# Performance work log

Measured on AMD Instinct MI355X. Metric: run time of the kernel, lower is better.

## Reference

```python
import jax, jax.numpy as jnp
import numpy as np

LAMBDA_COORD = 5.0
LAMBDA_NOOBJ = 0.5
CELL_SILE = 1.0 / 7.0


def setup_inputs() -> dict:
    key = jax.random.key(0)
    k1, k2, k3 = jax.random.split(key, 3)
    B, S, C = 16384, 49, 30
    predictions = jax.random.normal(k1, (B, S, C), dtype=jnp.float32)
    targets = jax.random.uniform(k2, (B, S, C), dtype=jnp.float32)
    # confidence column must be exactly 0/1 for the equality masks in the loss
    obj = (jax.random.uniform(k3, (B, S)) < 0.3).astype(jnp.float32)
    targets = targets.at[:, :, 4].set(obj)
    return {"predictions": predictions, "targets": targets}


def reference(predictions, targets):
    # Flatten cells: row-major order matches torch boolean indexing order.
    p = predictions.reshape(-1, 30)  # [N, 30], N = B*49
    t = targets.reshape(-1, 30)
    conf = t[:, 4]
    coord_mask = conf == 1.0
    noobj = (conf == 0.0).astype(p.dtype)

    # no-object confidence loss on columns [4, 9]
    noobj_loss = LAMBDA_NOOBJ * jnp.sum(
        noobj * ((p[:, 4] - t[:, 4]) ** 2 + (p[:, 9] - t[:, 9]) ** 2))

    # The original zips N_obj rows against N_obj//2 output rows, so only the
    # first floor(N_obj/2) object cells (in flattened order) contribute.
    n_obj = jnp.sum(coord_mask.astype(jnp.int32))
    rank = jnp.cumsum(coord_mask.astype(jnp.int32))  # 1-indexed object rank
    w = (coord_mask & (rank <= n_obj // 2)).astype(p.dtype)

    # pred boxes: columns [0:4] and [5:9] -> [N, 2, 4]
    pb = p[:, :10].reshape(-1, 2, 5)[..., :4]
    # faithful in-place transform: a = xy*c - wh ; b = a*c + wh
    pa = pb[..., :2] * CELL_SILE - pb[..., 2:4]
    pbb = pa * CELL_SILE + pb[..., 2:4]
    pbox = jnp.concatenate([pa, pbb], axis=-1)  # [N, 2, 4]

    tb = jnp.square(t[:, :4])
    ta = tb[:, :2] * CELL_SILE - tb[:, 2:4]
    tbb = ta * CELL_SILE + tb[:, 2:4]
    tbox = jnp.concatenate([ta, tbb], axis=-1)  # [N, 4]

    # torchvision.ops.box_iou, batched over cells
    lt = jnp.maximum(pbox[..., :2], tbox[:, None, :2])
    rb = jnp.minimum(pbox[..., 2:], tbox[:, None, 2:])
    whd = jnp.clip(rb - lt, 0.0)
    inter = whd[..., 0] * whd[..., 1]  # [N, 2]
    area_p = (pbox[..., 2] - pbox[..., 0]) * (pbox[..., 3] - pbox[..., 1])
    area_t = (tbox[:, 2] - tbox[:, 0]) * (tbox[:, 3] - tbox[:, 1])
    iou = inter / (area_p + area_t[:, None] - inter)  # [N, 2]

    idx = jnp.argmax(iou, axis=1)  # responsible box per cell
    sel = jnp.take_along_axis(p[:, :10].reshape(-1, 2, 5),
                              idx[:, None, None], axis=1)[:, 0, :]  # [N, 5]
    obj_idx = jnp.argmax(t[:, 10:], axis=1)
    sel_cls = jnp.take_along_axis(p[:, 10:], obj_idx[:, None], axis=1)[:, 0]

    center = jnp.sum(w * jnp.sum((sel[:, :2] - t[:, :2]) ** 2, axis=1))
    xywh = jnp.sum(w * jnp.sum((sel[:, 2:4] - t[:, 2:4]) ** 2, axis=1))
    # original compares column 5 twice (confidence_loss and classier_loss are
    # the same term): pred class prob vs constant 1
    conf_l = jnp.sum(w * (sel_cls - 1.0) ** 2)
    cls_l = jnp.sum(w * (sel_cls - 1.0) ** 2)

    return LAMBDA_COORD * (center + xywh + conf_l + cls_l) + noobj_loss
```

## Files before the change

kernel.cpp:

```cpp
#include <hip/hip_runtime.h>


#define COLS 30
#define NB   3136

typedef float f32x4 __attribute__((ext_vector_type(4)));
typedef float f32x2 __attribute__((ext_vector_type(2)));

#define ROW_MATH_BODY                                                        \
    const float C = 1.0f / 7.0f;                                             \
    float conf = b2.x;                         \
    coord = (conf == 1.0f);                                                  \
    noo = 0.0f;                                                              \
    if (conf == 0.0f) {                                                      \
        float d4_ = a2.x - conf;                                             \
        float d9_ = a4.y - b4.y;                                             \
        noo = d4_ * d4_ + d9_ * d9_;                                         \
    }                                                                        \
    float T0 = b0.x, T1 = b0.y, T2v = b1.x, T3 = b1.y;                       \
    float tb0 = T0 * T0, tb1 = T1 * T1, tb2 = T2v * T2v, tb3 = T3 * T3;      \
    float tax = tb0 * C - tb2, tay = tb1 * C - tb3;                          \
    float tbx = tax * C + tb2, tby = tay * C + tb3;                          \
    float areaT = (tbx - tax) * (tby - tay);                                 \
    float pax0 = a0.x * C - a1.x, pay0 = a0.y * C - a1.y;                    \
    float pbx0 = pax0 * C + a1.x, pby0 = pay0 * C + a1.y;                    \
    float pax1 = a2.y * C - a3.y, pay1 = a3.x * C - a4.x;                    \
    float pbx1 = pax1 * C + a3.y, pby1 = pay1 * C + a4.x;                    \
    float ltx = fmaxf(pax0, tax), lty = fmaxf(pay0, tay);                    \
    float rbx = fminf(pbx0, tbx), rby = fminf(pby0, tby);                    \
    float wx = fmaxf(rbx - ltx, 0.0f), wy = fmaxf(rby - lty, 0.0f);          \
    float inter = wx * wy;                                                   \
    float areaP = (pbx0 - pax0) * (pby0 - pay0);                             \
    float iou0 = inter / (areaP + areaT - inter);                            \
    ltx = fmaxf(pax1, tax); lty = fmaxf(pay1, tay);                          \
    rbx = fminf(pbx1, tbx); rby = fminf(pby1, tby);                          \
    wx = fmaxf(rbx - ltx, 0.0f); wy = fmaxf(rby - lty, 0.0f);                \
    inter = wx * wy;                                                         \
    areaP = (pbx1 - pax1) * (pby1 - pay1);                                   \
    float iou1 = inter / (areaP + areaT - inter);                            \
    int idx = (iou1 > iou0) ? 1 : 0;              \
    float sx = idx ? a2.y : a0.x;                                            \
    float sy = idx ? a3.x : a0.y;                                            \
    float sw = idx ? a3.y : a1.x;                                            \
    float sh = idx ? a4.x : a1.y;                                            \
    float best = b5.x, pc = a5.x;                \
    CLS_STEP(b5.y,  a5.y)  CLS_STEP(b6.x,  a6.x)  CLS_STEP(b6.y,  a6.y)      \
    CLS_STEP(b7.x,  a7.x)  CLS_STEP(b7.y,  a7.y)  CLS_STEP(b8.x,  a8.x)      \
    CLS_STEP(b8.y,  a8.y)  CLS_STEP(b9.x,  a9.x)  CLS_STEP(b9.y,  a9.y)      \
    CLS_STEP(b10.x, a10.x) CLS_STEP(b10.y, a10.y) CLS_STEP(b11.x, a11.x)     \
    CLS_STEP(b11.y, a11.y) CLS_STEP(b12.x, a12.x) CLS_STEP(b12.y, a12.y)     \
    CLS_STEP(b13.x, a13.x) CLS_STEP(b13.y, a13.y) CLS_STEP(b14.x, a14.x)     \
    CLS_STEP(b14.y, a14.y)                                                   \
    float d0 = sx - T0, d1 = sy - T1, d2 = sw - T2v, d3 = sh - T3;           \
    float dc = pc - 1.0f;                                                    \
    r = d0 * d0 + d1 * d1 + d2 * d2 + d3 * d3 + 2.0f * dc * dc;

#define CLS_STEP(tv, pv) { float v_ = (tv); if (v_ > best) { best = v_; pc = (pv); } }

__device__ __forceinline__ void row_compute_vals(
    float2 a0, float2 a1, float2 a2, float2 a3, float2 a4,
    float2 a5, float2 a6, float2 a7, float2 a8, float2 a9,
    float2 a10, float2 a11, float2 a12, float2 a13, float2 a14,
    float2 b0, float2 b1, float2 b2, float2 b3, float2 b4,
    float2 b5, float2 b6, float2 b7, float2 b8, float2 b9,
    float2 b10, float2 b11, float2 b12, float2 b13, float2 b14,
    bool& coord, float& r, float& noo)
{
    ROW_MATH_BODY
}

__device__ __forceinline__ void row_load_compute(
    const float* __restrict__ gp, const float* __restrict__ gt, long row,
    bool& coord, float& r, float& noo)
{
    const float2* P2 = (const float2*)(gp + row * (long)COLS);
    const float2* T2 = (const float2*)(gt + row * (long)COLS);
    float2 a0 = P2[0],  a1 = P2[1],  a2 = P2[2],  a3 = P2[3],  a4 = P2[4];
    float2 a5 = P2[5],  a6 = P2[6],  a7 = P2[7],  a8 = P2[8],  a9 = P2[9];
    float2 a10 = P2[10], a11 = P2[11], a12 = P2[12], a13 = P2[13], a14 = P2[14];
    float2 b0 = T2[0],  b1 = T2[1],  b2 = T2[2],  b3 = T2[3],  b4 = T2[4];
    float2 b5 = T2[5],  b6 = T2[6],  b7 = T2[7],  b8 = T2[8],  b9 = T2[9];
    float2 b10 = T2[10], b11 = T2[11], b12 = T2[12], b13 = T2[13], b14 = T2[14];
    ROW_MATH_BODY
}

__global__ __launch_bounds__(256, 2) void yolo_k1(const float* __restrict__ gp,
                                                  const float* __restrict__ gt,
                                                  int* __restrict__ cnt,
                                                  float* __restrict__ sumR,
                                                  float* __restrict__ noo) {
    __shared__ f32x4 ldsP[1920];
    __shared__ f32x4 ldsT[1920];
    __shared__ float wr[4], wn[4];
    __shared__ int wc[4];
    int tid = threadIdx.x;

    long gbase = (long)blockIdx.x * (256L * COLS);
    const float* gpb = gp + gbase;
    const float* gtb = gt + gbase;

    unsigned o0 = (unsigned)tid * 16u + 4096u;
    unsigned o1 = (unsigned)tid * 16u + 12288u;
    unsigned o2 = (unsigned)tid * 16u + 20480u;
    unsigned o3 = (unsigned)tid * 16u + 24576u;
    unsigned o4 = (unsigned)tid * 8u  + 28672u;

    f32x4 p0, p1, p2, p3, p4, p5, p6; f32x2 p7;
    f32x4 t0, t1, t2, t3, t4, t5, t6; f32x2 t7;
    asm volatile(
        "global_load_dwordx4 %0,  %[o0], %[pb] offset:-4096\n\t"
        "global_load_dwordx4 %1,  %[o0], %[pb]\n\t"
        "global_load_dwordx4 %2,  %[o1], %[pb] offset:-4096\n\t"
        "global_load_dwordx4 %3,  %[o1], %[pb]\n\t"
        "global_load_dwordx4 %4,  %[o2], %[pb] offset:-4096\n\t"
        "global_load_dwordx4 %5,  %[o2], %[pb]\n\t"
        "global_load_dwordx4 %6,  %[o3], %[pb]\n\t"
        "global_load_dwordx2 %7,  %[o4], %[pb]\n\t"
        "global_load_dwordx4 %8,  %[o0], %[tb] offset:-4096\n\t"
        "global_load_dwordx4 %9,  %[o0], %[tb]\n\t"
        "global_load_dwordx4 %10, %[o1], %[tb] offset:-4096\n\t"
        "global_load_dwordx4 %11, %[o1], %[tb]\n\t"
        "global_load_dwordx4 %12, %[o2], %[tb] offset:-4096\n\t"
        "global_load_dwordx4 %13, %[o2], %[tb]\n\t"
        "global_load_dwordx4 %14, %[o3], %[tb]\n\t"
        "global_load_dwordx2 %15, %[o4], %[tb]\n\t"
        "s_waitcnt vmcnt(0)"
        : "=&v"(p0), "=&v"(p1), "=&v"(p2), "=&v"(p3), "=&v"(p4), "=&v"(p5),
          "=&v"(p6), "=&v"(p7),
          "=&v"(t0), "=&v"(t1), "=&v"(t2), "=&v"(t3), "=&v"(t4), "=&v"(t5),
          "=&v"(t6), "=&v"(t7)
        : [o0]"v"(o0), [o1]"v"(o1), [o2]"v"(o2), [o3]"v"(o3), [o4]"v"(o4),
          [pb]"s"(gpb), [tb]"s"(gtb)
        : "memory");

    ldsP[0 * 256 + tid] = p0;  ldsP[1 * 256 + tid] = p1;
    ldsP[2 * 256 + tid] = p2;  ldsP[3 * 256 + tid] = p3;
    ldsP[4 * 256 + tid] = p4;  ldsP[5 * 256 + tid] = p5;
    ldsP[6 * 256 + tid] = p6;
    ldsT[0 * 256 + tid] = t0;  ldsT[1 * 256 + tid] = t1;
    ldsT[2 * 256 + tid] = t2;  ldsT[3 * 256 + tid] = t3;
    ldsT[4 * 256 + tid] = t4;  ldsT[5 * 256 + tid] = t5;
    ldsT[6 * 256 + tid] = t6;
    float* lpf = (float*)ldsP;
    float* ltf = (float*)ldsT;
    *(f32x2*)(lpf + 7168 + 2 * tid) = p7;
    *(f32x2*)(ltf + 7168 + 2 * tid) = t7;
    __syncthreads();

    const float2* P2 = (const float2*)(lpf + tid * COLS);
    const float2* T2 = (const float2*)(ltf + tid * COLS);
    float2 a0 = P2[0],  a1 = P2[1],  a2 = P2[2],  a3 = P2[3],  a4 = P2[4];
    float2 a5 = P2[5],  a6 = P2[6],  a7 = P2[7],  a8 = P2[8],  a9 = P2[9];
    float2 a10 = P2[10], a11 = P2[11], a12 = P2[12], a13 = P2[13], a14 = P2[14];
    float2 b0 = T2[0],  b1 = T2[1],  b2 = T2[2],  b3 = T2[3],  b4 = T2[4];
    float2 b5 = T2[5],  b6 = T2[6],  b7 = T2[7],  b8 = T2[8],  b9 = T2[9];
    float2 b10 = T2[10], b11 = T2[11], b12 = T2[12], b13 = T2[13], b14 = T2[14];

    bool coord; float r, nt;
    row_compute_vals(a0, a1, a2, a3, a4, a5, a6, a7, a8, a9,
                     a10, a11, a12, a13, a14,
                     b0, b1, b2, b3, b4, b5, b6, b7, b8, b9,
                     b10, b11, b12, b13, b14, coord, r, nt);
    float rl = coord ? r : 0.0f;

    unsigned long long bal = __ballot(coord);
    int c = (int)__popcll(bal);
#pragma unroll
    for (int off = 32; off > 0; off >>= 1) {
        rl += __shfl_down(rl, off);
        nt += __shfl_down(nt, off);
    }
    int wave = tid >> 6, lane = tid & 63;
    if (lane == 0) { wr[wave] = rl; wn[wave] = nt; wc[wave] = c; }
    __syncthreads();
    if (tid == 0) {
        cnt[blockIdx.x]  = wc[0] + wc[1] + wc[2] + wc[3];
        sumR[blockIdx.x] = wr[0] + wr[1] + wr[2] + wr[3];
        noo[blockIdx.x]  = wn[0] + wn[1] + wn[2] + wn[3];
    }
}

__global__ __launch_bounds__(256) void yolo_k2(const int* __restrict__ cnt,
                                               const float* __restrict__ sumR,
                                               const float* __restrict__ noo,
                                               const float* __restrict__ gp,
                                               const float* __restrict__ gt,
                                               float* __restrict__ out) {
    __shared__ int   wsum[4];
    __shared__ float wf[4], wn2[4];
    __shared__ int   s_bstar, s_kstar;
    __shared__ float s_base;
    __shared__ int   s_wcnt[4];
    int tid = threadIdx.x;
    int lane = tid & 63, wave = tid >> 6;
    if (tid == 0) { s_bstar = -1; s_kstar = 0; }

    const int PER = 13;
    int start = tid * PER;
    int end = min(NB, start + PER);

    int cloc = 0; float nloc = 0.0f;
    for (int i = start; i < end; ++i) { cloc += cnt[i]; nloc += noo[i]; }

    int incl = cloc;
#pragma unroll
    for (int off = 1; off < 64; off <<= 1) {
        int v = __shfl_up(incl, off);
        if (lane >= off) incl += v;
    }
    if (lane == 63) wsum[wave] = incl;
    __syncthreads();
    int woff = 0;
#pragma unroll
    for (int w = 0; w < 4; ++w) woff += (w < wave) ? wsum[w] : 0;
    int ex = woff + incl - cloc;
    int n_obj = wsum[0] + wsum[1] + wsum[2] + wsum[3];
    int n_half = n_obj >> 1;

    float acc = 0.0f;
    int running = ex;
    for (int i = start; i < end; ++i) {
        int ci = cnt[i];
        if (ci > 0) {
            if (running + ci <= n_half) {
                acc += sumR[i];
            } else if (running < n_half) {
                s_bstar = i;
                s_kstar = n_half - running;
            }
        }
        running += ci;
    }

#pragma unroll
    for (int off = 32; off > 0; off >>= 1) {
        acc  += __shfl_down(acc, off);
        nloc += __shfl_down(nloc, off);
    }
    if (lane == 0) { wf[wave] = acc; wn2[wave] = nloc; }
    __syncthreads();
    if (tid == 0)
        s_base = 5.0f * (wf[0] + wf[1] + wf[2] + wf[3])
               + 0.5f * (wn2[0] + wn2[1] + wn2[2] + wn2[3]);
    __syncthreads();

    int bstar = s_bstar, kstar = s_kstar;
    float total = 0.0f;
    if (bstar >= 0) {
        long row = (long)bstar * 256 + tid;
        bool coord; float r, nt;
        row_load_compute(gp, gt, row, coord, r, nt);
        unsigned long long bal = __ballot(coord);
        if (lane == 0) s_wcnt[wave] = (int)__popcll(bal);
        __syncthreads();
        int waveoff = 0;
#pragma unroll
        for (int w = 0; w < 4; ++w) waveoff += (w < wave) ? s_wcnt[w] : 0;
        unsigned long long below_incl =
            (lane == 63) ? bal : (bal & ((1ull << (lane + 1)) - 1ull));
        int rank = waveoff + (int)__popcll(below_incl);
        float val = (coord && rank <= kstar) ? r : 0.0f;
#pragma unroll
        for (int off = 32; off > 0; off >>= 1) val += __shfl_down(val, off);
        if (lane == 0) wf[wave] = val;
        __syncthreads();
        if (tid == 0) total = wf[0] + wf[1] + wf[2] + wf[3];
    }
    if (tid == 0) out[0] = s_base + 5.0f * total;
}

extern "C" void kernel_launch(void* const* d_in, const int* in_sizes, int n_in,
                              void* d_out, int out_size, void* d_ws, size_t ws_size,
                              hipStream_t stream) {
    (void)in_sizes; (void)n_in; (void)out_size; (void)ws_size;
    const float* p = (const float*)d_in[0];
    const float* t = (const float*)d_in[1];
    char* ws = (char*)d_ws;
    int*   cnt  = (int*)ws;
    float* sumR = (float*)(ws + (size_t)NB * 4);
    float* noo  = (float*)(ws + (size_t)NB * 8);
    float* out  = (float*)d_out;

    yolo_k1<<<NB, 256, 0, stream>>>(p, t, cnt, sumR, noo);
    yolo_k2<<<1, 256, 0, stream>>>(cnt, sumR, noo, p, t, out);
}
```

Before: 209.5 us.

## Make first-pass kernel persistent with register double-buffered tile prefetch

Launches a fixed grid of blocks that stride over the row tiles instead of one block per tile. Each block issues the global loads for its next tile into registers while it computes on the current tile from LDS, overlapping memory latency with compute. The cost is more live registers and an extra barrier per tile. A fixed grid of 512 blocks may also underfill the GPU or leave load imbalance, since 3136 tiles do not divide evenly across it.

```diff
diff --git a/kernel.cpp b/kernel.cpp
--- a/kernel.cpp
+++ b/kernel.cpp
@@ -3,6 +3,7 @@
 
 #define COLS 30
 #define NB   3136
+#define PB   512
 
 typedef float f32x4 __attribute__((ext_vector_type(4)));
 typedef float f32x2 __attribute__((ext_vector_type(2)));
@@ -84,6 +85,51 @@
     ROW_MATH_BODY
 }
 
+#define STAGE_ISSUE(gpb_, gtb_)                                              \
+    asm volatile(                                                            \
+        "global_load_dwordx4 %0,  %[o0], %[pb] offset:-4096\n\t"             \
+        "global_load_dwordx4 %1,  %[o0], %[pb]\n\t"                          \
+        "global_load_dwordx4 %2,  %[o1], %[pb] offset:-4096\n\t"             \
+        "global_load_dwordx4 %3,  %[o1], %[pb]\n\t"                          \
+        "global_load_dwordx4 %4,  %[o2], %[pb] offset:-4096\n\t"             \
+        "global_load_dwordx4 %5,  %[o2], %[pb]\n\t"                          \
+        "global_load_dwordx4 %6,  %[o3], %[pb]\n\t"                          \
+        "global_load_dwordx2 %7,  %[o4], %[pb]\n\t"                          \
+        "global_load_dwordx4 %8,  %[o0], %[tb] offset:-4096\n\t"             \
+        "global_load_dwordx4 %9,  %[o0], %[tb]\n\t"                          \
+        "global_load_dwordx4 %10, %[o1], %[tb] offset:-4096\n\t"             \
+        "global_load_dwordx4 %11, %[o1], %[tb]\n\t"                          \
+        "global_load_dwordx4 %12, %[o2], %[tb] offset:-4096\n\t"             \
+        "global_load_dwordx4 %13, %[o2], %[tb]\n\t"                          \
+        "global_load_dwordx4 %14, %[o3], %[tb]\n\t"                          \
+        "global_load_dwordx2 %15, %[o4], %[tb]\n\t"                          \
+        : "=&v"(p0), "=&v"(p1), "=&v"(p2), "=&v"(p3), "=&v"(p4), "=&v"(p5),  \
+          "=&v"(p6), "=&v"(p7),                                              \
+          "=&v"(q0), "=&v"(q1), "=&v"(q2), "=&v"(q3), "=&v"(q4), "=&v"(q5),  \
+          "=&v"(q6), "=&v"(q7)                                               \
+        : [o0]"v"(o0), [o1]"v"(o1), [o2]"v"(o2), [o3]"v"(o3), [o4]"v"(o4),   \
+          [pb]"s"(gpb_), [tb]"s"(gtb_)                                       \
+        : "memory")
+
+#define STAGE_WAIT()                                                         \
+    asm volatile("s_waitcnt vmcnt(0)"                                        \
+        : "+v"(p0), "+v"(p1), "+v"(p2), "+v"(p3), "+v"(p4), "+v"(p5),        \
+          "+v"(p6), "+v"(p7),                                                \
+          "+v"(q0), "+v"(q1), "+v"(q2), "+v"(q3), "+v"(q4), "+v"(q5),        \
+          "+v"(q6), "+v"(q7))
+
+#define STAGE_TO_LDS()                                                       \
+    ldsP[0 * 256 + tid] = p0;  ldsP[1 * 256 + tid] = p1;                     \
+    ldsP[2 * 256 + tid] = p2;  ldsP[3 * 256 + tid] = p3;                     \
+    ldsP[4 * 256 + tid] = p4;  ldsP[5 * 256 + tid] = p5;                     \
+    ldsP[6 * 256 + tid] = p6;                                                \
+    ldsT[0 * 256 + tid] = q0;  ldsT[1 * 256 + tid] = q1;                     \
+    ldsT[2 * 256 + tid] = q2;  ldsT[3 * 256 + tid] = q3;                     \
+    ldsT[4 * 256 + tid] = q4;  ldsT[5 * 256 + tid] = q5;                     \
+    ldsT[6 * 256 + tid] = q6;                                                \
+    *(f32x2*)(lpf + 7168 + 2 * tid) = p7;                                    \
+    *(f32x2*)(ltf + 7168 + 2 * tid) = q7;
+
 __global__ __launch_bounds__(256, 2) void yolo_k1(const float* __restrict__ gp,
                                                   const float* __restrict__ gt,
                                                   int* __restrict__ cnt,
@@ -94,10 +140,9 @@
     __shared__ float wr[4], wn[4];
     __shared__ int wc[4];
     int tid = threadIdx.x;
-
-    long gbase = (long)blockIdx.x * (256L * COLS);
-    const float* gpb = gp + gbase;
-    const float* gtb = gt + gbase;
+    int wave = tid >> 6, lane = tid & 63;
+    float* lpf = (float*)ldsP;
+    float* ltf = (float*)ldsT;
 
     unsigned o0 = (unsigned)tid * 16u + 4096u;
     unsigned o1 = (unsigned)tid * 16u + 12288u;
@@ -106,77 +151,64 @@
     unsigned o4 = (unsigned)tid * 8u  + 28672u;
 
     f32x4 p0, p1, p2, p3, p4, p5, p6; f32x2 p7;
-    f32x4 t0, t1, t2, t3, t4, t5, t6; f32x2 t7;
-    asm volatile(
-        "global_load_dwordx4 %0,  %[o0], %[pb] offset:-4096\n\t"
-        "global_load_dwordx4 %1,  %[o0], %[pb]\n\t"
-        "global_load_dwordx4 %2,  %[o1], %[pb] offset:-4096\n\t"
-        "global_load_dwordx4 %3,  %[o1], %[pb]\n\t"
-        "global_load_dwordx4 %4,  %[o2], %[pb] offset:-4096\n\t"
-        "global_load_dwordx4 %5,  %[o2], %[pb]\n\t"
-        "global_load_dwordx4 %6,  %[o3], %[pb]\n\t"
-        "global_load_dwordx2 %7,  %[o4], %[pb]\n\t"
-        "global_load_dwordx4 %8,  %[o0], %[tb] offset:-4096\n\t"
-        "global_load_dwordx4 %9,  %[o0], %[tb]\n\t"
-        "global_load_dwordx4 %10, %[o1], %[tb] offset:-4096\n\t"
-        "global_load_dwordx4 %11, %[o1], %[tb]\n\t"
-        "global_load_dwordx4 %12, %[o2], %[tb] offset:-4096\n\t"
-        "global_load_dwordx4 %13, %[o2], %[tb]\n\t"
-        "global_load_dwordx4 %14, %[o3], %[tb]\n\t"
-        "global_load_dwordx2 %15, %[o4], %[tb]\n\t"
-        "s_waitcnt vmcnt(0)"
-        : "=&v"(p0), "=&v"(p1), "=&v"(p2), "=&v"(p3), "=&v"(p4), "=&v"(p5),
-          "=&v"(p6), "=&v"(p7),
-          "=&v"(t0), "=&v"(t1), "=&v"(t2), "=&v"(t3), "=&v"(t4), "=&v"(t5),
-          "=&v"(t6), "=&v"(t7)
-        : [o0]"v"(o0), [o1]"v"(o1), [o2]"v"(o2), [o3]"v"(o3), [o4]"v"(o4),
-          [pb]"s"(gpb), [tb]"s"(gtb)
-        : "memory");
-
-    ldsP[0 * 256 + tid] = p0;  ldsP[1 * 256 + tid] = p1;
-    ldsP[2 * 256 + tid] = p2;  ldsP[3 * 256 + tid] = p3;
-    ldsP[4 * 256 + tid] = p4;  ldsP[5 * 256 + tid] = p5;
-    ldsP[6 * 256 + tid] = p6;
-    ldsT[0 * 256 + tid] = t0;  ldsT[1 * 256 + tid] = t1;
-    ldsT[2 * 256 + tid] = t2;  ldsT[3 * 256 + tid] = t3;
-    ldsT[4 * 256 + tid] = t4;  ldsT[5 * 256 + tid] = t5;
-    ldsT[6 * 256 + tid] = t6;
-    float* lpf = (float*)ldsP;
-    float* ltf = (float*)ldsT;
-    *(f32x2*)(lpf + 7168 + 2 * tid) = p7;
-    *(f32x2*)(ltf + 7168 + 2 * tid) = t7;
+    f32x4 q0, q1, q2, q3, q4, q5, q6; f32x2 q7;
+
+    int tt = blockIdx.x;
+    {
+        const float* gpb = gp + (long)tt * (256L * COLS);
+        const float* gtb = gt + (long)tt * (256L * COLS);
+        STAGE_ISSUE(gpb, gtb);
+        STAGE_WAIT();
+        STAGE_TO_LDS();
+    }
     __syncthreads();
 
-    const float2* P2 = (const float2*)(lpf + tid * COLS);
-    const float2* T2 = (const float2*)(ltf + tid * COLS);
-    float2 a0 = P2[0],  a1 = P2[1],  a2 = P2[2],  a3 = P2[3],  a4 = P2[4];
-    float2 a5 = P2[5],  a6 = P2[6],  a7 = P2[7],  a8 = P2[8],  a9 = P2[9];
-    float2 a10 = P2[10], a11 = P2[11], a12 = P2[12], a13 = P2[13], a14 = P2[14];
-    float2 b0 = T2[0],  b1 = T2[1],  b2 = T2[2],  b3 = T2[3],  b4 = T2[4];
-    float2 b5 = T2[5],  b6 = T2[6],  b7 = T2[7],  b8 = T2[8],  b9 = T2[9];
-    float2 b10 = T2[10], b11 = T2[11], b12 = T2[12], b13 = T2[13], b14 = T2[14];
-
-    bool coord; float r, nt;
-    row_compute_vals(a0, a1, a2, a3, a4, a5, a6, a7, a8, a9,
-                     a10, a11, a12, a13, a14,
-                     b0, b1, b2, b3, b4, b5, b6, b7, b8, b9,
-                     b10, b11, b12, b13, b14, coord, r, nt);
-    float rl = coord ? r : 0.0f;
-
-    unsigned long long bal = __ballot(coord);
-    int c = (int)__popcll(bal);
-#pragma unroll
-    for (int off = 32; off > 0; off >>= 1) {
-        rl += __shfl_down(rl, off);
-        nt += __shfl_down(nt, off);
-    }
-    int wave = tid >> 6, lane = tid & 63;
-    if (lane == 0) { wr[wave] = rl; wn[wave] = nt; wc[wave] = c; }
-    __syncthreads();
-    if (tid == 0) {
-        cnt[blockIdx.x]  = wc[0] + wc[1] + wc[2] + wc[3];
-        sumR[blockIdx.x] = wr[0] + wr[1] + wr[2] + wr[3];
-        noo[blockIdx.x]  = wn[0] + wn[1] + wn[2] + wn[3];
+    for (;;) {
+        int nt_tile = tt + PB;
+        bool have_next = nt_tile < NB;
+        if (have_next) {
+            const float* gpb = gp + (long)nt_tile * (256L * COLS);
+            const float* gtb = gt + (long)nt_tile * (256L * COLS);
+            STAGE_ISSUE(gpb, gtb);
+        }
+
+        {
+            const float2* P2 = (const float2*)(lpf + tid * COLS);
+            const float2* T2 = (const float2*)(ltf + tid * COLS);
+            float2 a0 = P2[0],  a1 = P2[1],  a2 = P2[2],  a3 = P2[3],  a4 = P2[4];
+            float2 a5 = P2[5],  a6 = P2[6],  a7 = P2[7],  a8 = P2[8],  a9 = P2[9];
+            float2 a10 = P2[10], a11 = P2[11], a12 = P2[12], a13 = P2[13], a14 = P2[14];
+            float2 b0 = T2[0],  b1 = T2[1],  b2 = T2[2],  b3 = T2[3],  b4 = T2[4];
+            float2 b5 = T2[5],  b6 = T2[6],  b7 = T2[7],  b8 = T2[8],  b9 = T2[9];
+            float2 b10 = T2[10], b11 = T2[11], b12 = T2[12], b13 = T2[13], b14 = T2[14];
+
+            bool coord; float r, nt;
+            row_compute_vals(a0, a1, a2, a3, a4, a5, a6, a7, a8, a9,
+                             a10, a11, a12, a13, a14,
+                             b0, b1, b2, b3, b4, b5, b6, b7, b8, b9,
+                             b10, b11, b12, b13, b14, coord, r, nt);
+            float rl = coord ? r : 0.0f;
+
+            unsigned long long bal = __ballot(coord);
+            int c = (int)__popcll(bal);
+#pragma unroll
+            for (int off = 32; off > 0; off >>= 1) {
+                rl += __shfl_down(rl, off);
+                nt += __shfl_down(nt, off);
+            }
+            if (lane == 0) { wr[wave] = rl; wn[wave] = nt; wc[wave] = c; }
+        }
+        __syncthreads();
+        if (tid == 0) {
+            cnt[tt]  = wc[0] + wc[1] + wc[2] + wc[3];
+            sumR[tt] = wr[0] + wr[1] + wr[2] + wr[3];
+            noo[tt]  = wn[0] + wn[1] + wn[2] + wn[3];
+        }
+        if (!have_next) break;
+        STAGE_WAIT();
+        STAGE_TO_LDS();
+        __syncthreads();
+        tt = nt_tile;
     }
 }
 
@@ -281,6 +313,6 @@
     float* noo  = (float*)(ws + (size_t)NB * 8);
     float* out  = (float*)d_out;
 
-    yolo_k1<<<NB, 256, 0, stream>>>(p, t, cnt, sumR, noo);
+    yolo_k1<<<PB, 256, 0, stream>>>(p, t, cnt, sumR, noo);
     yolo_k2<<<1, 256, 0, stream>>>(cnt, sumR, noo, p, t, out);
 }
```

Measured after the change: 209.7 us. Within noise of the previous version (+0.1%).
